# Optimization experiments

Hardware: AMD Instinct MI355X
Metric: run time of the kernel (lower is better)

Reference implementation:

```python
import jax, jax.numpy as jnp
import numpy as np

B, L, H, HEADS = 32, 512, 1024, 16
LN_EPS = 1e-5
NEG_INF = -1e9


def _layernorm(x, g, b):
    m = jnp.mean(x, axis=-1, keepdims=True)
    v = jnp.mean(jnp.square(x - m), axis=-1, keepdims=True)
    return (x - m) * jax.lax.rsqrt(v + LN_EPS) * g + b


def setup_inputs() -> dict:
    key = jax.random.key(0)
    ks = jax.random.split(key, 10)
    # deterministic variable graph sizes -> padding mask with fixed total valid count
    lengths = L - (np.arange(B) % 16) * 8          # per-graph node counts
    mask_np = np.arange(L)[None, :] < lengths[:, None]   # [B, L] bool
    node_idx = np.nonzero(mask_np.reshape(-1))[0].astype(np.int32)  # [14464]
    s = 0.02
    inp = {
        "x_dense": jax.random.normal(ks[0], (B, L, H), jnp.float32),
        "batch_CLS": jax.random.normal(ks[1], (B, 1, H), jnp.float32),
        "mask": jnp.asarray(mask_np),
        "node_idx": jnp.asarray(node_idx),
        "WQ": jax.random.normal(ks[2], (H, H), jnp.float32) * s,
        "bQ": jnp.zeros((H,), jnp.float32),
        "WK": jax.random.normal(ks[3], (H, H), jnp.float32) * s,
        "bK": jnp.zeros((H,), jnp.float32),
        "WV": jax.random.normal(ks[4], (H, H), jnp.float32) * s,
        "bV": jnp.zeros((H,), jnp.float32),
        "WO": jax.random.normal(ks[5], (H, H), jnp.float32) * s,
        "bO": jnp.zeros((H,), jnp.float32),
        "g1": jnp.ones((H,), jnp.float32),
        "beta1": jnp.zeros((H,), jnp.float32),
        "Wf1": jax.random.normal(ks[6], (H, 2 * H), jnp.float32) * s,
        "bf1": jnp.zeros((2 * H,), jnp.float32),
        "Wf2": jax.random.normal(ks[7], (2 * H, H), jnp.float32) * s,
        "bf2": jnp.zeros((H,), jnp.float32),
        "g2": jnp.ones((H,), jnp.float32),
        "beta2": jnp.zeros((H,), jnp.float32),
    }
    return inp


def reference(x_dense, batch_CLS, mask, node_idx, WQ, bQ, WK, bK, WV, bV,
              WO, bO, g1, beta1, Wf1, bf1, Wf2, bf2, g2, beta2):
    b, l, h = x_dense.shape
    d = h // HEADS
    # append CLS token; attention mask gets an always-True CLS column
    xd = jnp.concatenate([x_dense, batch_CLS], axis=1)            # [B, S, H], S = L+1
    am = jnp.concatenate([mask, jnp.ones((b, 1), bool)], axis=1)  # [B, S]
    S = l + 1
    Qh = (xd @ WQ + bQ).reshape(b, S, HEADS, d)
    Kh = (xd @ WK + bK).reshape(b, S, HEADS, d)
    Vh = (xd @ WV + bV).reshape(b, S, HEADS, d)
    scores = jnp.einsum('bqhd,bkhd->bhqk', Qh, Kh) / jnp.sqrt(jnp.float32(d))
    # additive padding mask over keys (masked_attention=True, clustering=False)
    scores = scores + jnp.where(am, 0.0, NEG_INF)[:, None, None, :]
    A = jax.nn.softmax(scores, axis=-1)                           # [B, h, S, S]
    # torch layout: A_torch[hh*B + b] == A[b, hh] -> cls_attn [h*B, S]
    cls_attn = jax.lax.stop_gradient(
        jnp.transpose(A[:, :, -1, :], (1, 0, 2)).reshape(HEADS * b, S))
    ctx = jnp.einsum('bhqk,bkhd->bqhd', A, Vh).reshape(b, S, h)
    attn_out = ctx @ WO + bO + xd                                  # residual
    cls_rows = attn_out[:, -1, :]                                  # [B, H]
    nodes = attn_out[:, :-1, :].reshape(b * l, h)[node_idx]        # valid nodes packed
    packed = jnp.concatenate([nodes, cls_rows], axis=0)            # [Ntot+B, H]
    h1 = _layernorm(packed, g1, beta1)
    ffn = jax.nn.relu(h1 @ Wf1 + bf1) @ Wf2 + bf2
    out = _layernorm(ffn + h1, g2, beta2)
    return out, cls_attn
```

## Files before the change

kernel.cpp:

```cpp
#include <hip/hip_runtime.h>
#include <stdint.h>

typedef unsigned short ushort_t;
typedef __bf16 bf16x8 __attribute__((ext_vector_type(8)));
typedef float  f32x4  __attribute__((ext_vector_type(4)));
typedef unsigned short ushortx8 __attribute__((ext_vector_type(8)));

constexpr int CB  = 32;
constexpr int CL  = 512;
constexpr int CNH = 16;
constexpr int CDH = 64;
constexpr int CS  = 513;
constexpr int CNR = CB * CS;
constexpr int CVTS = 576;
constexpr int CST = 136;
constexpr int CVTN = CB * CNH * CDH * CVTS;
constexpr int CZC0 = 384;

__device__ __forceinline__ float bf2f(ushort_t u) {
  return __builtin_bit_cast(float, (uint32_t)u << 16);
}
__device__ __forceinline__ ushort_t f2bf(float f) {
  __bf16 h = (__bf16)f;
  return __builtin_bit_cast(ushort_t, h);
}

typedef __attribute__((address_space(1))) const unsigned int GU32;
typedef __attribute__((address_space(3))) unsigned int LU32;
__device__ __forceinline__ void gld16(const void* g, void* l) {
  __builtin_amdgcn_global_load_lds((GU32*)g, (LU32*)l, 16, 0, 0);
}

__global__ __launch_bounds__(256)
void k_prep(const float* __restrict__ WQ, const float* __restrict__ WK,
            const float* __restrict__ WV, const float* __restrict__ WO,
            const float* __restrict__ Wf1, const float* __restrict__ Wf2,
            ushort_t* __restrict__ Wqkvt, ushort_t* __restrict__ Wot,
            ushort_t* __restrict__ Wf1t, ushort_t* __restrict__ Wf2t,
            const float* __restrict__ bQ, const float* __restrict__ bK,
            const float* __restrict__ bV, float* __restrict__ bqkv,
            int* __restrict__ lens, int* __restrict__ starts,
            const int* __restrict__ node_idx, int nn,
            const float* __restrict__ xd, const float* __restrict__ cls,
            ushort_t* __restrict__ XDP, ushort_t* __restrict__ Vt, int nPack) {
  const int bid = blockIdx.x;
  const int t = threadIdx.x;
  if (bid == 8192) {
    for (int i = t; i < 3072; i += 256)
      bqkv[i] = (i < 1024) ? bQ[i] : (i < 2048 ? bK[i - 1024] : bV[i - 2048]);
    if (t < CB) {
      int bounds[2];
#pragma unroll
      for (int e = 0; e < 2; ++e) {
        int target = (t + e) << 9;
        int lo = 0, hi = nn;
        while (lo < hi) {
          int mid = (lo + hi) >> 1;
          if (node_idx[mid] < target) lo = mid + 1; else hi = mid;
        }
        bounds[e] = lo;
      }
      starts[t] = bounds[0];
      lens[t] = bounds[1] - bounds[0];
    }
    return;
  }
  if (bid > 8192) {
    int pb2 = bid - 8193;
    if (pb2 < nPack) {
      size_t e = ((size_t)pb2 * 256 + t) * 8;
      int p = (int)(e >> 10);
      int col = (int)(e & 1023);
      const float* src = (p < nn) ? (xd + ((size_t)node_idx[p] << 10) + col)
                                  : (cls + ((size_t)(p - nn) << 10) + col);
      float4 v0 = ((const float4*)src)[0];
      float4 v1 = ((const float4*)src)[1];
      ushortx8 o;
      o[0] = f2bf(v0.x); o[1] = f2bf(v0.y); o[2] = f2bf(v0.z); o[3] = f2bf(v0.w);
      o[4] = f2bf(v1.x); o[5] = f2bf(v1.y); o[6] = f2bf(v1.z); o[7] = f2bf(v1.w);
      *((ushortx8*)(XDP + e)) = o;
    } else {
      int zb = pb2 - nPack;
      const ushortx8 z = {0, 0, 0, 0, 0, 0, 0, 0};
      const int upr = (CVTS - CZC0) / 8;
      const int totalRows = CB * CNH * CDH;
#pragma unroll
      for (int i = 0; i < 4; ++i) {
        int u = (zb * 1024) + i * 256 + t;
        int row = u / upr, w = u - row * upr;
        if (row < totalRows)
          *((ushortx8*)(Vt + (size_t)row * CVTS + CZC0 + w * 8)) = z;
      }
    }
    return;
  }
  const float* in; ushort_t* out; int R, C, tx32, ty32;
  if (bid < 3072) {
    int which = bid >> 10, tt = bid & 1023;
    in = (which == 0) ? WQ : (which == 1 ? WK : WV);
    out = Wqkvt + (size_t)which * 1024 * 1024;
    R = 1024; C = 1024; tx32 = tt & 31; ty32 = tt >> 5;
  } else if (bid < 4096) {
    int tt = bid - 3072;
    in = WO; out = Wot; R = 1024; C = 1024; tx32 = tt & 31; ty32 = tt >> 5;
  } else if (bid < 6144) {
    int tt = bid - 4096;
    in = Wf1; out = Wf1t; R = 1024; C = 2048; tx32 = tt & 63; ty32 = tt >> 6;
  } else {
    int tt = bid - 6144;
    in = Wf2; out = Wf2t; R = 2048; C = 1024; tx32 = tt & 31; ty32 = tt >> 5;
  }
  __shared__ float tle[32][33];
  const int c0 = tx32 * 32, r0 = ty32 * 32;
  const int tx = t & 31, ty = t >> 5;
#pragma unroll
  for (int i = 0; i < 4; ++i) {
    int r = ty + i * 8;
    tle[r][tx] = in[(size_t)(r0 + r) * C + c0 + tx];
  }
  __syncthreads();
#pragma unroll
  for (int i = 0; i < 4; ++i) {
    int r = ty + i * 8;
    out[(size_t)(c0 + r) * R + r0 + tx] = f2bf(tle[tx][r]);
  }
}

template <int EPI>
__global__ __launch_bounds__(256, 2)
void k_gemm(const ushort_t* __restrict__ A, const ushort_t* __restrict__ Bt,
            int M, int N, int K,
            const float* __restrict__ pb,
            const ushort_t* __restrict__ pauxB,
            const int* __restrict__ nidx, const int* __restrict__ plens, int nn,
            ushort_t* __restrict__ outB0, ushort_t* __restrict__ outB1) {
  __shared__ __align__(16) ushort_t sh[128 * CST];
  ushort_t* As = sh;
  ushort_t* Bs = sh + 8192;
  const int tid = threadIdx.x;
  const int lane = tid & 63, wid = tid >> 6;
  const int wr = wid >> 1, wc = wid & 1;
  const int lm = lane & 15, lq = lane >> 4;
  const int m0 = blockIdx.y * 128, n0 = blockIdx.x * 128;

  f32x4 acc[4][4];
  const f32x4 z4 = {0.f, 0.f, 0.f, 0.f};
#pragma unroll
  for (int i = 0; i < 4; ++i)
#pragma unroll
    for (int j = 0; j < 4; ++j) acc[i][j] = z4;

  for (int kt = 0; kt < K; kt += 64) {
    __syncthreads();
#pragma unroll
    for (int it = 0; it < 4; ++it) {
      int c = it * 256 + tid;
      int r = c >> 3, jc = c & 7;
      int j = jc ^ (r & 7);
      int ra = m0 + r; if (ra > M - 1) ra = M - 1;
      gld16(A + (size_t)ra * K + kt + j * 8, As + (size_t)c * 8);
    }
#pragma unroll
    for (int it = 0; it < 4; ++it) {
      int c = it * 256 + tid;
      int r = c >> 3, jc = c & 7;
      int j = jc ^ (r & 7);
      gld16(Bt + (size_t)(n0 + r) * K + kt + j * 8, Bs + (size_t)c * 8);
    }
    __syncthreads();
#pragma unroll
    for (int kk = 0; kk < 2; ++kk) {
      bf16x8 af[4], bfr[4];
#pragma unroll
      for (int mi = 0; mi < 4; ++mi) {
        int R = wr * 64 + mi * 16 + lm;
        int u = R * 8 + ((kk * 4 + lq) ^ (R & 7));
        af[mi] = *reinterpret_cast<const bf16x8*>(As + u * 8);
      }
#pragma unroll
      for (int ni = 0; ni < 4; ++ni) {
        int R = wc * 64 + ni * 16 + lm;
        int u = R * 8 + ((kk * 4 + lq) ^ (R & 7));
        bfr[ni] = *reinterpret_cast<const bf16x8*>(Bs + u * 8);
      }
#pragma unroll
      for (int mi = 0; mi < 4; ++mi)
#pragma unroll
        for (int ni = 0; ni < 4; ++ni)
          acc[mi][ni] = __builtin_amdgcn_mfma_f32_16x16x32_bf16(af[mi], bfr[ni], acc[mi][ni], 0, 0, 0);
    }
  }

  __syncthreads();
  ushort_t* Cs = sh;
#pragma unroll
  for (int mi = 0; mi < 4; ++mi) {
#pragma unroll
    for (int ni = 0; ni < 4; ++ni) {
#pragma unroll
      for (int j = 0; j < 4; ++j) {
        int row = wr * 64 + mi * 16 + lq * 4 + j;
        int c128 = wc * 64 + ni * 16 + lm;
        int r = m0 + row;
        int rc = r < M ? r : M - 1;
        int c = n0 + c128;
        float v = acc[mi][ni][j] + pb[c];
        if constexpr (EPI == 1) v += bf2f(pauxB[(size_t)rc * 1024 + c]);
        else if constexpr (EPI == 2) v = v > 0.f ? v : 0.f;
        Cs[row * CST + c128] = f2bf(v);
      }
    }
  }
  __syncthreads();

  if (EPI == 0 && n0 >= 2048) {
    const int row = tid & 127;
    const int half = tid >> 7;
    const int r = m0 + row;
    if (r < M) {
      int b, s;
      if (r < nn) { int idx = nidx[r]; b = idx >> 9; s = idx & 511; }
      else        { b = r - nn; s = plens[b]; }
      const int cvbase = n0 - 2048;
#pragma unroll 8
      for (int ci = 0; ci < 64; ++ci) {
        int c128 = half * 64 + ci;
        int cv = cvbase + c128;
        int h = cv >> 6, d = cv & 63;
        outB1[((size_t)(b * CNH + h) * CDH + d) * CVTS + s] = Cs[row * CST + c128];
      }
    }
  } else {
    const int ld = (EPI == 1) ? 1024 : 2048;
#pragma unroll
    for (int it = 0; it < 8; ++it) {
      int g = it * 256 + tid;
      int row = g >> 4, c16 = g & 15;
      int r = m0 + row;
      if (r >= M) continue;
      ushortx8 val = *reinterpret_cast<const ushortx8*>(&Cs[row * CST + c16 * 8]);
      *reinterpret_cast<ushortx8*>(&outB0[(size_t)r * ld + n0 + c16 * 8]) = val;
    }
  }
}

__global__ __launch_bounds__(256, 2)
void k_attn(const ushort_t* __restrict__ QK, const ushort_t* __restrict__ Vt,
            const int* __restrict__ lens, const int* __restrict__ starts, int nn,
            ushort_t* __restrict__ CTX) {
  __shared__ __align__(16) ushort_t Ks[2][64 * 64];
  __shared__ __align__(16) ushort_t Vs[2][64 * 64];
  __shared__ __align__(16) ushort_t Ps[4][16][72];

  const int tid = threadIdx.x;
  const int lane = tid & 63, wid = tid >> 6;
  const int lm = lane & 15, lq = lane >> 4;

  const int bidx = blockIdx.x;
  const int qt = bidx >> 9;
  const int hb = bidx & 511;
  const int h = hb & 15, b = hb >> 4;
  const int len = lens[b];
  if (qt * 128 >= len) return;
  const int st0 = starts[b];
  const int clsrow = nn + b;

  const int qbase = qt * 128 + wid * 16;

  const int sr = tid >> 3, sjc = tid & 7;
  const int sj = sjc ^ (sr & 7);
  const size_t vtBase = (size_t)(b * CNH + h) * CDH * CVTS;

  bf16x8 aq[2][2];
#pragma unroll
  for (int t2 = 0; t2 < 2; ++t2) {
    int qr = qbase + t2 * 64 + lm; if (qr > len - 1) qr = len - 1;
    const ushort_t* qptr = QK + (size_t)(st0 + qr) * 2048 + h * CDH + lq * 8;
    aq[t2][0] = *reinterpret_cast<const bf16x8*>(qptr);
    aq[t2][1] = *reinterpret_cast<const bf16x8*>(qptr + 32);
  }

  const f32x4 z4 = {0.f, 0.f, 0.f, 0.f};
  f32x4 acc[2][4];
#pragma unroll
  for (int t2 = 0; t2 < 2; ++t2)
#pragma unroll
    for (int i = 0; i < 4; ++i) acc[t2][i] = z4;
  float lrow[2][4];
#pragma unroll
  for (int t2 = 0; t2 < 2; ++t2)
#pragma unroll
    for (int r2 = 0; r2 < 4; ++r2) lrow[t2][r2] = 0.f;

  const float C1 = 0.125f * 1.44269504f;
  const int NC = (len + 64) >> 6;

  {
    int k = sr;
    int krow = (k < len) ? (st0 + k) : clsrow;
    gld16(QK + (size_t)krow * 2048 + 1024 + h * CDH + sj * 8, Ks[0] + (size_t)tid * 8);
    gld16(QK + (size_t)(((32 + sr) < len) ? (st0 + 32 + sr) : clsrow) * 2048 + 1024 + h * CDH + sj * 8,
          Ks[0] + (size_t)(256 + tid) * 8);
    gld16(Vt + vtBase + (size_t)sr * CVTS + sj * 8, Vs[0] + (size_t)tid * 8);
    gld16(Vt + vtBase + (size_t)(32 + sr) * CVTS + sj * 8, Vs[0] + (size_t)(256 + tid) * 8);
  }
  __syncthreads();

  int cur = 0;
  for (int kc = 0; kc < NC; ++kc) {
    const int k0 = kc * 64;
    const bool full = (k0 + 64 <= len);

    if (kc + 1 < NC) {
      const int nk0 = k0 + 64;
      int nxt = cur ^ 1;
      int k1 = nk0 + sr;
      int k2 = nk0 + 32 + sr;
      int krow1 = (k1 < len) ? (st0 + k1) : clsrow;
      int krow2 = (k2 < len) ? (st0 + k2) : clsrow;
      gld16(QK + (size_t)krow1 * 2048 + 1024 + h * CDH + sj * 8, Ks[nxt] + (size_t)tid * 8);
      gld16(QK + (size_t)krow2 * 2048 + 1024 + h * CDH + sj * 8, Ks[nxt] + (size_t)(256 + tid) * 8);
      gld16(Vt + vtBase + (size_t)sr * CVTS + nk0 + sj * 8, Vs[nxt] + (size_t)tid * 8);
      gld16(Vt + vtBase + (size_t)(32 + sr) * CVTS + nk0 + sj * 8, Vs[nxt] + (size_t)(256 + tid) * 8);
    }

    const ushort_t* Kc = Ks[cur];
    const ushort_t* Vc = Vs[cur];

#pragma unroll
    for (int t2 = 0; t2 < 2; ++t2) {
      f32x4 sc[4];
#pragma unroll
      for (int st = 0; st < 4; ++st) sc[st] = z4;
#pragma unroll
      for (int kk = 0; kk < 2; ++kk) {
        bf16x8 kb[4];
#pragma unroll
        for (int st = 0; st < 4; ++st) {
          int R = st * 16 + lm;
          int u = R * 8 + ((kk * 4 + lq) ^ (R & 7));
          kb[st] = *reinterpret_cast<const bf16x8*>(Kc + u * 8);
        }
#pragma unroll
        for (int st = 0; st < 4; ++st)
          sc[st] = __builtin_amdgcn_mfma_f32_16x16x32_bf16(aq[t2][kk], kb[st], sc[st], 0, 0, 0);
      }

      if (full) {
#pragma unroll
        for (int st = 0; st < 4; ++st) {
#pragma unroll
          for (int r2 = 0; r2 < 4; ++r2) {
            float e = exp2f(sc[st][r2] * C1);
            lrow[t2][r2] += e;
            Ps[wid][lq * 4 + r2][st * 16 + lm] = f2bf(e);
          }
        }
      } else {
#pragma unroll
        for (int st = 0; st < 4; ++st) {
          int kg = k0 + st * 16 + lm;
          float madd = (kg <= len) ? 0.f : -1e9f;
#pragma unroll
          for (int r2 = 0; r2 < 4; ++r2) {
            float e = exp2f(__builtin_fmaf(sc[st][r2], C1, madd));
            lrow[t2][r2] += e;
            Ps[wid][lq * 4 + r2][st * 16 + lm] = f2bf(e);
          }
        }
      }

      bf16x8 ap[2];
      ap[0] = *reinterpret_cast<const bf16x8*>(&Ps[wid][lm][lq * 8]);
      ap[1] = *reinterpret_cast<const bf16x8*>(&Ps[wid][lm][32 + lq * 8]);
#pragma unroll
      for (int kk = 0; kk < 2; ++kk) {
#pragma unroll
        for (int dt = 0; dt < 4; ++dt) {
          int R = dt * 16 + lm;
          int u = R * 8 + ((kk * 4 + lq) ^ (R & 7));
          bf16x8 vb = *reinterpret_cast<const bf16x8*>(Vc + u * 8);
          acc[t2][dt] = __builtin_amdgcn_mfma_f32_16x16x32_bf16(ap[kk], vb, acc[t2][dt], 0, 0, 0);
        }
      }
    }

    __syncthreads();
    cur ^= 1;
  }

#pragma unroll
  for (int t2 = 0; t2 < 2; ++t2) {
    float inv[4];
#pragma unroll
    for (int r2 = 0; r2 < 4; ++r2) {
      float s0 = lrow[t2][r2];
      s0 += __shfl_xor(s0, 1);
      s0 += __shfl_xor(s0, 2);
      s0 += __shfl_xor(s0, 4);
      s0 += __shfl_xor(s0, 8);
      inv[r2] = 1.f / s0;
    }
#pragma unroll
    for (int dt = 0; dt < 4; ++dt) {
#pragma unroll
      for (int r2 = 0; r2 < 4; ++r2) {
        int q = qbase + t2 * 64 + lq * 4 + r2;
        if (q < len)
          CTX[(size_t)(st0 + q) * 1024 + h * CDH + dt * 16 + lm] = f2bf(acc[t2][dt][r2] * inv[r2]);
      }
    }
  }
}

__global__ __launch_bounds__(64)
void k_attn_cls(const ushort_t* __restrict__ QK, const ushort_t* __restrict__ Vt,
                const int* __restrict__ lens, const int* __restrict__ starts, int nn,
                ushort_t* __restrict__ CTX, float* __restrict__ clsOut) {
  const int bid = blockIdx.x;
  const int h = bid >> 5, b = bid & 31;
  const int l = threadIdx.x;
  __shared__ float qv[64];
  __shared__ float probs[516];
  const int st0 = starts[b];
  const int clsrow = nn + b;
  qv[l] = bf2f(QK[(size_t)clsrow * 2048 + h * CDH + l]);
  __syncthreads();
  const int len = lens[b];

  float sc[9];
  float mx = -INFINITY;
#pragma unroll
  for (int i = 0; i < 9; ++i) {
    int k = l + 64 * i;
    if (k < CS) {
      int krow = (k < len) ? (st0 + k) : clsrow;
      const ushort_t* kr = QK + (size_t)krow * 2048 + 1024 + h * CDH;
      float a2 = 0.f;
#pragma unroll
      for (int d0 = 0; d0 < 64; d0 += 8) {
        bf16x8 kv = *reinterpret_cast<const bf16x8*>(kr + d0);
#pragma unroll
        for (int j = 0; j < 8; ++j) a2 += qv[d0 + j] * (float)kv[j];
      }
      a2 *= 0.125f;
      if (!((k < len) || (k == 512))) a2 += -1e9f;
      sc[i] = a2;
      mx = fmaxf(mx, a2);
    } else {
      sc[i] = -INFINITY;
    }
  }
  for (int m2 = 1; m2 < 64; m2 <<= 1) mx = fmaxf(mx, __shfl_xor(mx, m2));
  float sum = 0.f, p[9];
#pragma unroll
  for (int i = 0; i < 9; ++i) { p[i] = __expf(sc[i] - mx); sum += p[i]; }
  for (int m2 = 1; m2 < 64; m2 <<= 1) sum += __shfl_xor(sum, m2);
  float invs = 1.f / sum;
#pragma unroll
  for (int i = 0; i < 9; ++i) {
    int k = l + 64 * i;
    if (k < CS) {
      float pr = p[i] * invs;
      clsOut[(size_t)bid * CS + k] = pr;
      probs[k] = pr;
    }
  }
  __syncthreads();
  const ushort_t* vr = Vt + ((size_t)(b * CNH + h) * CDH + l) * CVTS;
  float a2 = 0.f;
  for (int k = 0; k < 512; k += 8) {
    bf16x8 vv = *reinterpret_cast<const bf16x8*>(vr + k);
#pragma unroll
    for (int j = 0; j < 8; ++j) a2 += probs[k + j] * (float)vv[j];
  }
  a2 += probs[512] * bf2f(vr[len]);
  CTX[(size_t)clsrow * 1024 + h * CDH + l] = f2bf(a2);
}

template <int MODE>
__global__ __launch_bounds__(256)
void k_ln(const ushort_t* __restrict__ X,
          const float* __restrict__ g, const float* __restrict__ be,
          float* __restrict__ outF, ushort_t* __restrict__ outB) {
  const int p = blockIdx.x;
  const int t = threadIdx.x;
  const uint2 u = ((const uint2*)(X + (size_t)p * 1024))[t];
  float v0 = bf2f((ushort_t)(u.x & 0xffff)), v1 = bf2f((ushort_t)(u.x >> 16));
  float v2 = bf2f((ushort_t)(u.y & 0xffff)), v3 = bf2f((ushort_t)(u.y >> 16));
  float s1 = v0 + v1 + v2 + v3;
  float s2 = v0 * v0 + v1 * v1 + v2 * v2 + v3 * v3;
  for (int m2 = 1; m2 < 64; m2 <<= 1) {
    s1 += __shfl_xor(s1, m2);
    s2 += __shfl_xor(s2, m2);
  }
  __shared__ float red[8];
  const int lane = t & 63, wid = t >> 6;
  if (lane == 0) { red[wid] = s1; red[4 + wid] = s2; }
  __syncthreads();
  s1 = red[0] + red[1] + red[2] + red[3];
  s2 = red[4] + red[5] + red[6] + red[7];
  float mean = s1 * (1.f / 1024.f);
  float var = s2 * (1.f / 1024.f) - mean * mean;
  float rs = rsqrtf(var + 1e-5f);
  float4 gv = ((const float4*)g)[t];
  float4 bv = ((const float4*)be)[t];
  float y0 = (v0 - mean) * rs * gv.x + bv.x;
  float y1 = (v1 - mean) * rs * gv.y + bv.y;
  float y2 = (v2 - mean) * rs * gv.z + bv.z;
  float y3 = (v3 - mean) * rs * gv.w + bv.w;
  if constexpr (MODE == 0) {
    uint2 o;
    o.x = (unsigned)f2bf(y0) | ((unsigned)f2bf(y1) << 16);
    o.y = (unsigned)f2bf(y2) | ((unsigned)f2bf(y3) << 16);
    ((uint2*)(outB + (size_t)p * 1024))[t] = o;
  } else {
    ((float4*)(outF + (size_t)p * 1024))[t] = make_float4(y0, y1, y2, y3);
  }
}

extern "C" void kernel_launch(void* const* d_in, const int* in_sizes, int n_in,
                              void* d_out, int out_size, void* d_ws, size_t ws_size,
                              hipStream_t stream) {
  const float* x_dense = (const float*)d_in[0];
  const float* bcls    = (const float*)d_in[1];
  const int*   node_idx = (const int*)d_in[3];
  const float* WQ = (const float*)d_in[4];
  const float* bQ = (const float*)d_in[5];
  const float* WK = (const float*)d_in[6];
  const float* bK = (const float*)d_in[7];
  const float* WV = (const float*)d_in[8];
  const float* bV = (const float*)d_in[9];
  const float* WO = (const float*)d_in[10];
  const float* bO = (const float*)d_in[11];
  const float* g1 = (const float*)d_in[12];
  const float* be1 = (const float*)d_in[13];
  const float* Wf1 = (const float*)d_in[14];
  const float* bf1 = (const float*)d_in[15];
  const float* Wf2 = (const float*)d_in[16];
  const float* bf2 = (const float*)d_in[17];
  const float* g2 = (const float*)d_in[18];
  const float* be2 = (const float*)d_in[19];

  const int nn = in_sizes[3];
  const int NP = nn + CB;

  char* ws = (char*)d_ws;
  const size_t oWqkv = 0;
  const size_t oWo   = oWqkv + (size_t)3072 * 1024 * 2;
  const size_t oWf1  = oWo + (size_t)1024 * 1024 * 2;
  const size_t oWf2  = oWf1 + (size_t)2048 * 1024 * 2;
  const size_t oBqkv = oWf2 + (size_t)1024 * 2048 * 2;
  const size_t oLens = oBqkv + 3072 * 4;
  const size_t oRA = (oLens + 512 + 255) & ~(size_t)255;
  const size_t szRA = (size_t)CNR * 2048 * 2;
  const size_t oRB = oRA + szRA;
  const size_t szRB = (size_t)CNR * 1024 * 2;
  const size_t oRC = oRB + szRB;
  const size_t szVt = (size_t)CVTN * 2;
  const size_t oRD = oRC + szVt;

  ushort_t* Wqkvt = (ushort_t*)(ws + oWqkv);
  ushort_t* Wot   = (ushort_t*)(ws + oWo);
  ushort_t* Wf1t  = (ushort_t*)(ws + oWf1);
  ushort_t* Wf2t  = (ushort_t*)(ws + oWf2);
  float* bqkv = (float*)(ws + oBqkv);
  int* lens   = (int*)(ws + oLens);
  int* starts = lens + CB;
  ushort_t* QK  = (ushort_t*)(ws + oRA);
  ushort_t* CTX = (ushort_t*)(ws + oRB);
  ushort_t* Vt  = (ushort_t*)(ws + oRC);
  ushort_t* XDP = (ushort_t*)(ws + oRD);
  ushort_t* AO  = (ushort_t*)(ws + oRA);
  ushort_t* H1B = (ushort_t*)(ws + oRB);
  ushort_t* G   = (ushort_t*)(ws + oRA);
  ushort_t* F   = (ushort_t*)(ws + oRC);

  float* out0 = (float*)d_out;
  float* clsOut = out0 + (size_t)NP * 1024;

  dim3 blk(256);
  const int nPack = NP / 2;
  const int totalZU = (CB * CNH * CDH) * ((CVTS - CZC0) / 8);
  const int nZero = (totalZU + 1023) / 1024;
  k_prep<<<dim3(8193 + nPack + nZero), blk, 0, stream>>>(
      WQ, WK, WV, WO, Wf1, Wf2, Wqkvt, Wot, Wf1t, Wf2t,
      bQ, bK, bV, bqkv, lens, starts, node_idx, nn, x_dense, bcls, XDP, Vt, nPack);

  const int mtP = (NP + 127) / 128;
  k_gemm<0><<<dim3(3072 / 128, mtP), blk, 0, stream>>>(
      XDP, Wqkvt, NP, 3072, 1024, bqkv, nullptr, node_idx, lens, nn, QK, Vt);
  k_attn<<<dim3(CB * CNH * 4), blk, 0, stream>>>(QK, Vt, lens, starts, nn, CTX);
  k_attn_cls<<<dim3(CB * CNH), dim3(64), 0, stream>>>(QK, Vt, lens, starts, nn, CTX, clsOut);
  k_gemm<1><<<dim3(1024 / 128, mtP), blk, 0, stream>>>(
      CTX, Wot, NP, 1024, 1024, bO, XDP, nullptr, nullptr, nn, AO, nullptr);
  k_ln<0><<<dim3(NP), blk, 0, stream>>>(AO, g1, be1, nullptr, H1B);
  k_gemm<2><<<dim3(2048 / 128, mtP), blk, 0, stream>>>(
      H1B, Wf1t, NP, 2048, 1024, bf1, nullptr, nullptr, nullptr, nn, G, nullptr);
  k_gemm<1><<<dim3(1024 / 128, mtP), blk, 0, stream>>>(
      G, Wf2t, NP, 1024, 2048, bf2, H1B, nullptr, nullptr, nn, F, nullptr);
  k_ln<1><<<dim3(NP), blk, 0, stream>>>(F, g2, be2, out0, nullptr);
  (void)ws_size; (void)out_size; (void)n_in;
}
```

Baseline: 436.2 us.

## Halve GEMM epilogue LDS footprint and fold CLS attention into main attention kernel

The GEMM epilogue now stages the output tile through shared memory in two 64-row halves, which shrinks the LDS allocation from 128*136 to 16384 elements so more blocks can be resident. The separate CLS-attention kernel is merged into k_attn as 128 extra blocks, each wave handling one (batch, head) CLS row, which removes one launch. In exchange the epilogue needs extra barriers, and the CLS path relies on wave-local LDS without a barrier between the writes and reads of q/probs.

After: 460.9 us. 5.7% more time.

```diff
diff --git a/kernel.cpp b/kernel.cpp
--- a/kernel.cpp
+++ b/kernel.cpp
@@ -134,7 +134,7 @@
             const ushort_t* __restrict__ pauxB,
             const int* __restrict__ nidx, const int* __restrict__ plens, int nn,
             ushort_t* __restrict__ outB0, ushort_t* __restrict__ outB1) {
-  __shared__ __align__(16) ushort_t sh[128 * CST];
+  __shared__ __align__(16) ushort_t sh[16384];
   ushort_t* As = sh;
   ushort_t* Bs = sh + 8192;
   const int tid = threadIdx.x;
@@ -191,55 +191,59 @@
     }
   }
 
-  __syncthreads();
   ushort_t* Cs = sh;
 #pragma unroll
-  for (int mi = 0; mi < 4; ++mi) {
-#pragma unroll
-    for (int ni = 0; ni < 4; ++ni) {
-#pragma unroll
-      for (int j = 0; j < 4; ++j) {
-        int row = wr * 64 + mi * 16 + lq * 4 + j;
-        int c128 = wc * 64 + ni * 16 + lm;
-        int r = m0 + row;
-        int rc = r < M ? r : M - 1;
-        int c = n0 + c128;
-        float v = acc[mi][ni][j] + pb[c];
-        if constexpr (EPI == 1) v += bf2f(pauxB[(size_t)rc * 1024 + c]);
-        else if constexpr (EPI == 2) v = v > 0.f ? v : 0.f;
-        Cs[row * CST + c128] = f2bf(v);
-      }
-    }
-  }
-  __syncthreads();
-
-  if (EPI == 0 && n0 >= 2048) {
-    const int row = tid & 127;
-    const int half = tid >> 7;
-    const int r = m0 + row;
-    if (r < M) {
-      int b, s;
-      if (r < nn) { int idx = nidx[r]; b = idx >> 9; s = idx & 511; }
-      else        { b = r - nn; s = plens[b]; }
-      const int cvbase = n0 - 2048;
+  for (int hf = 0; hf < 2; ++hf) {
+    __syncthreads();
+    if (wr == hf) {
+#pragma unroll
+      for (int mi = 0; mi < 4; ++mi) {
+#pragma unroll
+        for (int ni = 0; ni < 4; ++ni) {
+#pragma unroll
+          for (int j = 0; j < 4; ++j) {
+            int rowl = mi * 16 + lq * 4 + j;
+            int c128 = wc * 64 + ni * 16 + lm;
+            int r = m0 + hf * 64 + rowl;
+            int rc = r < M ? r : M - 1;
+            int c = n0 + c128;
+            float v = acc[mi][ni][j] + pb[c];
+            if constexpr (EPI == 1) v += bf2f(pauxB[(size_t)rc * 1024 + c]);
+            else if constexpr (EPI == 2) v = v > 0.f ? v : 0.f;
+            Cs[rowl * CST + c128] = f2bf(v);
+          }
+        }
+      }
+    }
+    __syncthreads();
+    if (EPI == 0 && n0 >= 2048) {
+      const int rowl = tid & 63;
+      const int qtr = tid >> 6;
+      const int r = m0 + hf * 64 + rowl;
+      if (r < M) {
+        int b, s;
+        if (r < nn) { int idx = nidx[r]; b = idx >> 9; s = idx & 511; }
+        else        { b = r - nn; s = plens[b]; }
+        const int cvbase = n0 - 2048;
 #pragma unroll 8
-      for (int ci = 0; ci < 64; ++ci) {
-        int c128 = half * 64 + ci;
-        int cv = cvbase + c128;
-        int h = cv >> 6, d = cv & 63;
-        outB1[((size_t)(b * CNH + h) * CDH + d) * CVTS + s] = Cs[row * CST + c128];
-      }
-    }
-  } else {
-    const int ld = (EPI == 1) ? 1024 : 2048;
-#pragma unroll
-    for (int it = 0; it < 8; ++it) {
-      int g = it * 256 + tid;
-      int row = g >> 4, c16 = g & 15;
-      int r = m0 + row;
-      if (r >= M) continue;
-      ushortx8 val = *reinterpret_cast<const ushortx8*>(&Cs[row * CST + c16 * 8]);
-      *reinterpret_cast<ushortx8*>(&outB0[(size_t)r * ld + n0 + c16 * 8]) = val;
+        for (int ci = 0; ci < 32; ++ci) {
+          int c128 = qtr * 32 + ci;
+          int cv = cvbase + c128;
+          int h = cv >> 6, d = cv & 63;
+          outB1[((size_t)(b * CNH + h) * CDH + d) * CVTS + s] = Cs[rowl * CST + c128];
+        }
+      }
+    } else {
+      const int ld = (EPI == 1) ? 1024 : 2048;
+#pragma unroll
+      for (int it = 0; it < 4; ++it) {
+        int g = it * 256 + tid;
+        int rowl = g >> 4, c16 = g & 15;
+        int r = m0 + hf * 64 + rowl;
+        if (r >= M) continue;
+        ushortx8 val = *reinterpret_cast<const ushortx8*>(&Cs[rowl * CST + c16 * 8]);
+        *reinterpret_cast<ushortx8*>(&outB0[(size_t)r * ld + n0 + c16 * 8]) = val;
+      }
     }
   }
 }
@@ -247,7 +251,7 @@
 __global__ __launch_bounds__(256, 2)
 void k_attn(const ushort_t* __restrict__ QK, const ushort_t* __restrict__ Vt,
             const int* __restrict__ lens, const int* __restrict__ starts, int nn,
-            ushort_t* __restrict__ CTX) {
+            ushort_t* __restrict__ CTX, float* __restrict__ clsOut) {
   __shared__ __align__(16) ushort_t Ks[2][64 * 64];
   __shared__ __align__(16) ushort_t Vs[2][64 * 64];
   __shared__ __align__(16) ushort_t Ps[4][16][72];
@@ -255,8 +259,69 @@
   const int tid = threadIdx.x;
   const int lane = tid & 63, wid = tid >> 6;
   const int lm = lane & 15, lq = lane >> 4;
-
   const int bidx = blockIdx.x;
+
+  if (bidx >= 2048) {
+    const int idx4 = ((bidx - 2048) << 2) | wid;
+    const int h = idx4 >> 5, b = idx4 & 31;
+    const int l = lane;
+    float* qv = (float*)(Ks[0]) + wid * 640;
+    float* probs = qv + 64;
+    const int st0 = starts[b];
+    const int clsrow = nn + b;
+    qv[l] = bf2f(QK[(size_t)clsrow * 2048 + h * CDH + l]);
+    const int len = lens[b];
+
+    float sc[9];
+    float mx = -INFINITY;
+#pragma unroll
+    for (int i = 0; i < 9; ++i) {
+      int k = l + 64 * i;
+      if (k < CS) {
+        int krow = (k < len) ? (st0 + k) : clsrow;
+        const ushort_t* kr = QK + (size_t)krow * 2048 + 1024 + h * CDH;
+        float a2 = 0.f;
+#pragma unroll
+        for (int d0 = 0; d0 < 64; d0 += 8) {
+          bf16x8 kv = *reinterpret_cast<const bf16x8*>(kr + d0);
+#pragma unroll
+          for (int j = 0; j < 8; ++j) a2 += qv[d0 + j] * (float)kv[j];
+        }
+        a2 *= 0.125f;
+        if (!((k < len) || (k == 512))) a2 += -1e9f;
+        sc[i] = a2;
+        mx = fmaxf(mx, a2);
+      } else {
+        sc[i] = -INFINITY;
+      }
+    }
+    for (int m2 = 1; m2 < 64; m2 <<= 1) mx = fmaxf(mx, __shfl_xor(mx, m2));
+    float sum = 0.f, p[9];
+#pragma unroll
+    for (int i = 0; i < 9; ++i) { p[i] = __expf(sc[i] - mx); sum += p[i]; }
+    for (int m2 = 1; m2 < 64; m2 <<= 1) sum += __shfl_xor(sum, m2);
+    float invs = 1.f / sum;
+#pragma unroll
+    for (int i = 0; i < 9; ++i) {
+      int k = l + 64 * i;
+      if (k < CS) {
+        float pr = p[i] * invs;
+        clsOut[(size_t)idx4 * CS + k] = pr;
+        probs[k] = pr;
+      }
+    }
+    const ushort_t* vr = Vt + ((size_t)(b * CNH + h) * CDH + l) * CVTS;
+    float a2 = 0.f;
+    for (int k = 0; k < 512; k += 8) {
+      bf16x8 vv = *reinterpret_cast<const bf16x8*>(vr + k);
+#pragma unroll
+      for (int j = 0; j < 8; ++j) a2 += probs[k + j] * (float)vv[j];
+    }
+    a2 += probs[512] * bf2f(vr[len]);
+    CTX[(size_t)clsrow * 1024 + h * CDH + l] = f2bf(a2);
+    return;
+  }
+
   const int qt = bidx >> 9;
   const int hb = bidx & 511;
   const int h = hb & 15, b = hb >> 4;
@@ -296,8 +361,7 @@
   const int NC = (len + 64) >> 6;
 
   {
-    int k = sr;
-    int krow = (k < len) ? (st0 + k) : clsrow;
+    int krow = (sr < len) ? (st0 + sr) : clsrow;
     gld16(QK + (size_t)krow * 2048 + 1024 + h * CDH + sj * 8, Ks[0] + (size_t)tid * 8);
     gld16(QK + (size_t)(((32 + sr) < len) ? (st0 + 32 + sr) : clsrow) * 2048 + 1024 + h * CDH + sj * 8,
           Ks[0] + (size_t)(256 + tid) * 8);
@@ -411,71 +475,6 @@
       }
     }
   }
-}
-
-__global__ __launch_bounds__(64)
-void k_attn_cls(const ushort_t* __restrict__ QK, const ushort_t* __restrict__ Vt,
-                const int* __restrict__ lens, const int* __restrict__ starts, int nn,
-                ushort_t* __restrict__ CTX, float* __restrict__ clsOut) {
-  const int bid = blockIdx.x;
-  const int h = bid >> 5, b = bid & 31;
-  const int l = threadIdx.x;
-  __shared__ float qv[64];
-  __shared__ float probs[516];
-  const int st0 = starts[b];
-  const int clsrow = nn + b;
-  qv[l] = bf2f(QK[(size_t)clsrow * 2048 + h * CDH + l]);
-  __syncthreads();
-  const int len = lens[b];
-
-  float sc[9];
-  float mx = -INFINITY;
-#pragma unroll
-  for (int i = 0; i < 9; ++i) {
-    int k = l + 64 * i;
-    if (k < CS) {
-      int krow = (k < len) ? (st0 + k) : clsrow;
-      const ushort_t* kr = QK + (size_t)krow * 2048 + 1024 + h * CDH;
-      float a2 = 0.f;
-#pragma unroll
-      for (int d0 = 0; d0 < 64; d0 += 8) {
-        bf16x8 kv = *reinterpret_cast<const bf16x8*>(kr + d0);
-#pragma unroll
-        for (int j = 0; j < 8; ++j) a2 += qv[d0 + j] * (float)kv[j];
-      }
-      a2 *= 0.125f;
-      if (!((k < len) || (k == 512))) a2 += -1e9f;
-      sc[i] = a2;
-      mx = fmaxf(mx, a2);
-    } else {
-      sc[i] = -INFINITY;
-    }
-  }
-  for (int m2 = 1; m2 < 64; m2 <<= 1) mx = fmaxf(mx, __shfl_xor(mx, m2));
-  float sum = 0.f, p[9];
-#pragma unroll
-  for (int i = 0; i < 9; ++i) { p[i] = __expf(sc[i] - mx); sum += p[i]; }
-  for (int m2 = 1; m2 < 64; m2 <<= 1) sum += __shfl_xor(sum, m2);
-  float invs = 1.f / sum;
-#pragma unroll
-  for (int i = 0; i < 9; ++i) {
-    int k = l + 64 * i;
-    if (k < CS) {
-      float pr = p[i] * invs;
-      clsOut[(size_t)bid * CS + k] = pr;
-      probs[k] = pr;
-    }
-  }
-  __syncthreads();
-  const ushort_t* vr = Vt + ((size_t)(b * CNH + h) * CDH + l) * CVTS;
-  float a2 = 0.f;
-  for (int k = 0; k < 512; k += 8) {
-    bf16x8 vv = *reinterpret_cast<const bf16x8*>(vr + k);
-#pragma unroll
-    for (int j = 0; j < 8; ++j) a2 += probs[k + j] * (float)vv[j];
-  }
-  a2 += probs[512] * bf2f(vr[len]);
-  CTX[(size_t)clsrow * 1024 + h * CDH + l] = f2bf(a2);
 }
 
 template <int MODE>
@@ -590,8 +589,7 @@
   const int mtP = (NP + 127) / 128;
   k_gemm<0><<<dim3(3072 / 128, mtP), blk, 0, stream>>>(
       XDP, Wqkvt, NP, 3072, 1024, bqkv, nullptr, node_idx, lens, nn, QK, Vt);
-  k_attn<<<dim3(CB * CNH * 4), blk, 0, stream>>>(QK, Vt, lens, starts, nn, CTX);
-  k_attn_cls<<<dim3(CB * CNH), dim3(64), 0, stream>>>(QK, Vt, lens, starts, nn, CTX, clsOut);
+  k_attn<<<dim3(CB * CNH * 4 + 128), blk, 0, stream>>>(QK, Vt, lens, starts, nn, CTX, clsOut);
   k_gemm<1><<<dim3(1024 / 128, mtP), blk, 0, stream>>>(
       CTX, Wot, NP, 1024, 1024, bO, XDP, nullptr, nullptr, nn, AO, nullptr);
   k_ln<0><<<dim3(NP), blk, 0, stream>>>(AO, g1, be1, nullptr, H1B);
```
